# Optimization experiments

Measured on AMD Instinct MI355X. Metric: run time of the kernel, lower is better.

Reference implementation:

```python
import jax, jax.numpy as jnp
import numpy as np

VOCAB, EMBED, HIDDEN, NCLS, PAD = 50257, 512, 1024, 4, 0

def setup_inputs() -> dict:
    key = jax.random.key(0)
    k1, k2, k3, k4, k5, k6 = jax.random.split(key, 6)
    emb = jax.random.uniform(k1, (VOCAB, EMBED), jnp.float32, -0.1, 0.1)
    emb = emb.at[PAD].set(0.0)
    W = jax.random.normal(k2, (HIDDEN, EMBED), jnp.float32) * (2.0 / (EMBED + HIDDEN)) ** 0.5
    b_w = jnp.zeros((HIDDEN,), jnp.float32)
    U = jax.random.normal(k3, (HIDDEN, HIDDEN), jnp.float32) * (1.0 / HIDDEN) ** 0.5
    V = jax.random.normal(k4, (NCLS, HIDDEN), jnp.float32) * (2.0 / (HIDDEN + NCLS)) ** 0.5
    b_v = jnp.zeros((NCLS,), jnp.float32)
    x = jax.random.randint(k5, (64, 512), 0, VOCAB, jnp.int32)
    return {"x": x, "emb": emb, "W": W, "b_w": b_w, "U": U, "V": V, "b_v": b_v}

def reference(x, emb, W, b_w, U, V, b_v):
    # x: [B, S] int tokens. Dropouts are identity (eval mode).
    embedded = emb[x]                      # [B, S, E]
    # Precompute Wx for all timesteps in one GEMM: [B, S, H]
    wx = jnp.einsum('bse,he->bsh', embedded, W) + b_w
    B = x.shape[0]
    h0 = jnp.zeros((B, W.shape[0]), embedded.dtype)

    def step(h, wx_t):
        h = jnp.tanh(wx_t + h @ U.T)       # [B, H]
        return h, None

    h_final, _ = jax.lax.scan(step, h0, jnp.swapaxes(wx, 0, 1))  # scan over S
    return h_final @ V.T + b_v             # [B, NCLS]
```

## Files before the change

kernel.cpp:

```cpp
#include <hip/hip_runtime.h>
#include <stdint.h>

#define B 64
#define S 512
#define E 512
#define H 1024
#define NCLS 4

typedef __attribute__((ext_vector_type(8))) short short8;
typedef __attribute__((ext_vector_type(4))) float f32x4;

__device__ __forceinline__ unsigned short f32_to_bf16(float f) {
    unsigned int x = __float_as_uint(f);
    unsigned int r = (x + 0x7fffu + ((x >> 16) & 1u)) >> 16;
    return (unsigned short)r;
}
__device__ __forceinline__ float bf16_to_f32(unsigned short u) {
    return __uint_as_float(((unsigned int)u) << 16);
}

__device__ __forceinline__ void store_sc4u(unsigned int* p, unsigned int v) {
    asm volatile("global_store_dword %0, %1, off sc0 sc1"
                 :: "v"(p), "v"(v) : "memory");
}

#define K1_LDA 40

__global__ __launch_bounds__(256) void k_wx_gemm(
    const int* __restrict__ x, const float* __restrict__ emb,
    const float* __restrict__ W, const float* __restrict__ bw,
    unsigned short* __restrict__ wx)
{
    __shared__ unsigned short Asub[128 * K1_LDA];
    __shared__ unsigned short Bsub[128 * K1_LDA];

    const int t  = threadIdx.x;
    const int mt = blockIdx.x;
    const int nt = blockIdx.y;
    const int i0 = mt * 128;
    const int j0 = nt * 128;

    const int r  = t >> 1;
    const int kh = (t & 1) * 16;
    const int tok = x[i0 + r];
    const float* arow = emb + (size_t)tok * E;
    const float* brow = W + (size_t)(j0 + r) * E;

    const int lane = t & 63;
    const int w    = t >> 6;
    const int wm   = (w >> 1) * 64;
    const int wn   = (w & 1) * 64;
    const int fr   = lane & 15;
    const int kg   = lane >> 4;

    f32x4 acc[4][4] = {};

    for (int kt = 0; kt < E; kt += 32) {
        __syncthreads();
        {
            union { unsigned short us[8]; uint4 v; } p;
            const float* srcA = arow + kt + kh;
            #pragma unroll
            for (int i = 0; i < 8; ++i) p.us[i] = f32_to_bf16(srcA[i]);
            *(uint4*)&Asub[r * K1_LDA + kh] = p.v;
            #pragma unroll
            for (int i = 0; i < 8; ++i) p.us[i] = f32_to_bf16(srcA[8 + i]);
            *(uint4*)&Asub[r * K1_LDA + kh + 8] = p.v;
            const float* srcB = brow + kt + kh;
            #pragma unroll
            for (int i = 0; i < 8; ++i) p.us[i] = f32_to_bf16(srcB[i]);
            *(uint4*)&Bsub[r * K1_LDA + kh] = p.v;
            #pragma unroll
            for (int i = 0; i < 8; ++i) p.us[i] = f32_to_bf16(srcB[8 + i]);
            *(uint4*)&Bsub[r * K1_LDA + kh + 8] = p.v;
        }
        __syncthreads();

        short8 a[4], b[4];
        #pragma unroll
        for (int mi = 0; mi < 4; ++mi)
            a[mi] = *(const short8*)&Asub[(wm + mi * 16 + fr) * K1_LDA + kg * 8];
        #pragma unroll
        for (int ni = 0; ni < 4; ++ni)
            b[ni] = *(const short8*)&Bsub[(wn + ni * 16 + fr) * K1_LDA + kg * 8];
        #pragma unroll
        for (int mi = 0; mi < 4; ++mi)
            #pragma unroll
            for (int ni = 0; ni < 4; ++ni)
                acc[mi][ni] = __builtin_amdgcn_mfma_f32_16x16x32_bf16(
                                  a[mi], b[ni], acc[mi][ni], 0, 0, 0);
    }

    float bwv[4];
    #pragma unroll
    for (int ni = 0; ni < 4; ++ni) bwv[ni] = bw[j0 + wn + ni * 16 + fr];
    #pragma unroll
    for (int mi = 0; mi < 4; ++mi) {
        #pragma unroll
        for (int ni = 0; ni < 4; ++ni) {
            const int gn = j0 + wn + ni * 16 + fr;
            #pragma unroll
            for (int rr = 0; rr < 4; ++rr) {
                const int gm = i0 + wm + mi * 16 + kg * 4 + rr;
                const int bb = gm >> 9;
                const int ss = gm & 511;
                wx[(size_t)(ss * B + bb) * H + gn] =
                    f32_to_bf16(acc[mi][ni][rr] + bwv[ni]);
            }
        }
    }
}

__global__ __launch_bounds__(256) void k_rnn(
    const unsigned short* __restrict__ wx, const float* __restrict__ U,
    const float* __restrict__ Vw, const float* __restrict__ bv,
    unsigned int* __restrict__ hbuf, unsigned int* __restrict__ flags,
    float* __restrict__ out)
{
    __shared__ __align__(16) unsigned short Uhi[32 * 1024];
    __shared__ __align__(16) unsigned int Hh32[8 * 512];
    __shared__ __align__(16) unsigned int Hl32[8 * 512];
    __shared__ __align__(16) float redC[1024];

    const int t   = threadIdx.x;
    const int g   = blockIdx.x & 7;
    const int m   = blockIdx.x >> 3;
    const int j0  = m * 32;
    const int bg0 = g * 8;

    for (int rr = 0; rr < 32; ++rr) {
        f32x4 v = *(const f32x4*)(U + (size_t)(j0 + rr) * H + t * 4);
        uint2 hwd;
        hwd.x = f32_to_bf16(v[0]) | ((unsigned)f32_to_bf16(v[1]) << 16);
        hwd.y = f32_to_bf16(v[2]) | ((unsigned)f32_to_bf16(v[3]) << 16);
        const int byteoff = (rr * 2048 + t * 8) ^ ((rr & 7) << 4);
        *(uint2*)((char*)Uhi + byteoff) = hwd;
    }

    const int lane  = t & 63;
    const int w     = t >> 6;
    const int fr    = lane & 15;
    const int kg    = lane >> 4;
    const int kbase = w * 256;
    const int abrow = fr & 7;
    const int ob    = t >> 5;
    const int oj    = t & 31;

    unsigned int* fl = flags + g * 32;

    float wxv = bf16_to_f32(wx[(size_t)(bg0 + ob) * H + j0 + oj]);

    __syncthreads();

    for (int ts = 0; ts < S; ++ts) {
        const unsigned int* hr = hbuf + (ts & 1) * (B * H);
        unsigned int*       hw = hbuf + ((ts + 1) & 1) * (B * H);

        {
            const unsigned int* fp = fl + w * 8 + (lane & 7);
            unsigned int fv;
            do {
                fv = __hip_atomic_load(fp, __ATOMIC_RELAXED,
                                       __HIP_MEMORY_SCOPE_AGENT);
            } while (!__all((int)(fv >= (unsigned)ts)));
        }

        float wx_next = 0.f;
        if (ts + 1 < S)
            wx_next = bf16_to_f32(wx[(size_t)((ts + 1) * B + bg0 + ob) * H + j0 + oj]);

        {
            const unsigned long long* hb64 = (const unsigned long long*)hr;
            unsigned long long vv[16];
            #pragma unroll
            for (int i = 0; i < 16; ++i) {
                const int li = lane + 64 * i;
                const int b = li >> 7, col = li & 127;
                vv[i] = __hip_atomic_load(
                    hb64 + (size_t)(bg0 + b) * 512 + w * 128 + col,
                    __ATOMIC_RELAXED, __HIP_MEMORY_SCOPE_AGENT);
            }
            #pragma unroll
            for (int i = 0; i < 16; ++i) {
                const int li = lane + 64 * i;
                const int b = li >> 7;
                const int k2 = w * 128 + (li & 127);
                const unsigned int v0 = (unsigned int)vv[i];
                const unsigned int v1 = (unsigned int)(vv[i] >> 32);
                const int idx = (b * 512 + k2) ^ (b << 2);
                Hh32[idx] = (v0 >> 16) | (v1 & 0xffff0000u);
                Hl32[idx] = (v0 & 0xffffu) | (v1 << 16);
            }
        }

        f32x4 acc0 = {}, acc1 = {};
        #pragma unroll
        for (int kk = 0; kk < 8; ++kk) {
            const int k  = kbase + kk * 32 + kg * 8;
            const int ab = (abrow * 2048 + k * 2) ^ (abrow << 4);
            const short8 ahi = *(const short8*)((const char*)Hh32 + ab);
            const short8 alo = *(const short8*)((const char*)Hl32 + ab);
            const int b0 = (fr * 2048 + k * 2) ^ ((fr & 7) << 4);
            const int b1 = ((16 + fr) * 2048 + k * 2) ^ ((fr & 7) << 4);
            const short8 bh0 = *(const short8*)((const char*)Uhi + b0);
            const short8 bh1 = *(const short8*)((const char*)Uhi + b1);
            acc0 = __builtin_amdgcn_mfma_f32_16x16x32_bf16(ahi, bh0, acc0, 0, 0, 0);
            acc0 = __builtin_amdgcn_mfma_f32_16x16x32_bf16(alo, bh0, acc0, 0, 0, 0);
            acc1 = __builtin_amdgcn_mfma_f32_16x16x32_bf16(ahi, bh1, acc1, 0, 0, 0);
            acc1 = __builtin_amdgcn_mfma_f32_16x16x32_bf16(alo, bh1, acc1, 0, 0, 0);
        }

        if (kg < 2) {
            #pragma unroll
            for (int rr = 0; rr < 4; ++rr) {
                const int mb = kg * 4 + rr;
                redC[w * 256 + mb * 32 + fr]      = acc0[rr];
                redC[w * 256 + mb * 32 + 16 + fr] = acc1[rr];
            }
        }
        __syncthreads();

        float sum = redC[      ob * 32 + oj] + redC[256 + ob * 32 + oj]
                  + redC[512 + ob * 32 + oj] + redC[768 + ob * 32 + oj];

        float p = wxv + sum;
        p = fminf(fmaxf(p, -15.f), 15.f);
        const float e  = __expf(2.0f * p);
        const float hv = 1.0f - 2.0f / (e + 1.0f);

        const unsigned short hib = f32_to_bf16(hv);
        const unsigned short lob = f32_to_bf16(hv - bf16_to_f32(hib));
        store_sc4u(hw + (size_t)(bg0 + ob) * H + j0 + oj,
                   ((unsigned int)hib << 16) | lob);
        asm volatile("s_waitcnt vmcnt(0)" ::: "memory");
        __syncthreads();
        if (t == 0)
            __hip_atomic_store(&fl[m], (unsigned)(ts + 1), __ATOMIC_RELAXED,
                               __HIP_MEMORY_SCOPE_AGENT);
        wxv = wx_next;
    }

    if (m == 0) {
        if (t < 32)
            while (__hip_atomic_load(&fl[t], __ATOMIC_RELAXED,
                                     __HIP_MEMORY_SCOPE_AGENT) < (unsigned)S) {}
        __syncthreads();
        const unsigned int* hf = hbuf;
        const int o = t & 31, part = t >> 5;
        const int pb = o >> 2, c = o & 3;
        const unsigned long long* hrow =
            (const unsigned long long*)(hf + (size_t)(bg0 + pb) * H) + part * 64;
        const float* vrow = Vw + (size_t)c * H + part * 128;
        float partial = 0.f;
        for (int q = 0; q < 64; ++q) {
            unsigned long long vvq = __hip_atomic_load(hrow + q, __ATOMIC_RELAXED,
                                                       __HIP_MEMORY_SCOPE_AGENT);
            const unsigned int v0 = (unsigned int)vvq;
            const unsigned int v1 = (unsigned int)(vvq >> 32);
            const float h0 = bf16_to_f32((unsigned short)(v0 >> 16))
                           + bf16_to_f32((unsigned short)(v0 & 0xffffu));
            const float h1 = bf16_to_f32((unsigned short)(v1 >> 16))
                           + bf16_to_f32((unsigned short)(v1 & 0xffffu));
            partial += h0 * vrow[2 * q] + h1 * vrow[2 * q + 1];
        }
        __syncthreads();
        redC[part * 32 + o] = partial;
        __syncthreads();
        if (t < 32) {
            float sv = 0.f;
            #pragma unroll
            for (int pq = 0; pq < 8; ++pq) sv += redC[pq * 32 + t];
            out[(bg0 + (t >> 2)) * NCLS + (t & 3)] = sv + bv[t & 3];
        }
    }
}

extern "C" void kernel_launch(void* const* d_in, const int* in_sizes, int n_in,
                              void* d_out, int out_size, void* d_ws, size_t ws_size,
                              hipStream_t stream)
{
    const int*   x   = (const int*)d_in[0];
    const float* emb = (const float*)d_in[1];
    const float* W   = (const float*)d_in[2];
    const float* bw  = (const float*)d_in[3];
    const float* U   = (const float*)d_in[4];
    const float* V   = (const float*)d_in[5];
    const float* bv  = (const float*)d_in[6];
    float* out = (float*)d_out;

    unsigned short* wx = (unsigned short*)d_ws;
    const size_t WX_BYTES = (size_t)S * B * H * sizeof(unsigned short);
    unsigned int* hbuf = (unsigned int*)((char*)d_ws + WX_BYTES);
    const size_t HB_BYTES = (size_t)2 * B * H * sizeof(unsigned int);
    unsigned int* flags = (unsigned int*)((char*)d_ws + WX_BYTES + HB_BYTES);

    hipMemsetAsync((char*)d_ws + WX_BYTES, 0, HB_BYTES + 2048, stream);

    hipLaunchKernelGGL(k_wx_gemm, dim3(256, 8), dim3(256), 0, stream,
                       x, emb, W, bw, wx);
    hipLaunchKernelGGL(k_rnn, dim3(256), dim3(256), 0, stream,
                       wx, U, V, bv, hbuf, flags, out);
}
```

Baseline: 1.592 ms.

## Load hidden state directly into MFMA registers, skipping the LDS staging

Each step now reads the previous hidden state from global memory with 128-bit coherent loads straight into each lane's MFMA A-operand layout. The hi/lo bf16 halves are split in registers instead of being written to and read back from the Hh32/Hl32 shared buffers. The wx prefetch is moved ahead of the flag spin-wait so it overlaps the wait. A dummy LDS pad array is added, apparently to limit occupancy or block placement. The trade-off is that lanes with fr>=8 sit idle during the loads, and their A rows stay uninitialised.

Result: slower. 1.759 ms (+10.5%).

```diff
diff --git a/kernel.cpp b/kernel.cpp
--- a/kernel.cpp
+++ b/kernel.cpp
@@ -23,6 +23,10 @@
     asm volatile("global_store_dword %0, %1, off sc0 sc1"
                  :: "v"(p), "v"(v) : "memory");
 }
+
+#define LD128(dst, base, off) \
+    asm volatile("global_load_dwordx4 %0, %1, off offset:" #off " sc0 sc1" \
+                 : "=&v"(dst) : "v"(base) : "memory")
 
 #define K1_LDA 40
 
@@ -118,15 +122,16 @@
     float* __restrict__ out)
 {
     __shared__ __align__(16) unsigned short Uhi[32 * 1024];
-    __shared__ __align__(16) unsigned int Hh32[8 * 512];
-    __shared__ __align__(16) unsigned int Hl32[8 * 512];
     __shared__ __align__(16) float redC[1024];
+    __shared__ __align__(16) unsigned int pad_lds[8192];
 
     const int t   = threadIdx.x;
     const int g   = blockIdx.x & 7;
     const int m   = blockIdx.x >> 3;
     const int j0  = m * 32;
     const int bg0 = g * 8;
+
+    ((volatile unsigned int*)pad_lds)[t] = (unsigned int)t;
 
     for (int rr = 0; rr < 32; ++rr) {
         f32x4 v = *(const f32x4*)(U + (size_t)(j0 + rr) * H + t * 4);
@@ -156,6 +161,10 @@
         const unsigned int* hr = hbuf + (ts & 1) * (B * H);
         unsigned int*       hw = hbuf + ((ts + 1) & 1) * (B * H);
 
+        float wx_next = 0.f;
+        if (ts + 1 < S)
+            wx_next = bf16_to_f32(wx[(size_t)((ts + 1) * B + bg0 + ob) * H + j0 + oj]);
+
         {
             const unsigned int* fp = fl + w * 8 + (lane & 7);
             unsigned int fv;
@@ -165,49 +174,45 @@
             } while (!__all((int)(fv >= (unsigned)ts)));
         }
 
-        float wx_next = 0.f;
-        if (ts + 1 < S)
-            wx_next = bf16_to_f32(wx[(size_t)((ts + 1) * B + bg0 + ob) * H + j0 + oj]);
-
+        uint4 hv[16];
         {
-            const unsigned long long* hb64 = (const unsigned long long*)hr;
-            unsigned long long vv[16];
-            #pragma unroll
-            for (int i = 0; i < 16; ++i) {
-                const int li = lane + 64 * i;
-                const int b = li >> 7, col = li & 127;
-                vv[i] = __hip_atomic_load(
-                    hb64 + (size_t)(bg0 + b) * 512 + w * 128 + col,
-                    __ATOMIC_RELAXED, __HIP_MEMORY_SCOPE_AGENT);
+            const unsigned int* hb =
+                hr + (size_t)(bg0 + abrow) * H + kbase + kg * 8;
+            if (fr < 8) {
+                LD128(hv[ 0], hb,   0); LD128(hv[ 1], hb,  16);
+                LD128(hv[ 2], hb, 128); LD128(hv[ 3], hb, 144);
+                LD128(hv[ 4], hb, 256); LD128(hv[ 5], hb, 272);
+                LD128(hv[ 6], hb, 384); LD128(hv[ 7], hb, 400);
+                LD128(hv[ 8], hb, 512); LD128(hv[ 9], hb, 528);
+                LD128(hv[10], hb, 640); LD128(hv[11], hb, 656);
+                LD128(hv[12], hb, 768); LD128(hv[13], hb, 784);
+                LD128(hv[14], hb, 896); LD128(hv[15], hb, 912);
             }
-            #pragma unroll
-            for (int i = 0; i < 16; ++i) {
-                const int li = lane + 64 * i;
-                const int b = li >> 7;
-                const int k2 = w * 128 + (li & 127);
-                const unsigned int v0 = (unsigned int)vv[i];
-                const unsigned int v1 = (unsigned int)(vv[i] >> 32);
-                const int idx = (b * 512 + k2) ^ (b << 2);
-                Hh32[idx] = (v0 >> 16) | (v1 & 0xffff0000u);
-                Hl32[idx] = (v0 & 0xffffu) | (v1 << 16);
+            asm volatile("s_waitcnt vmcnt(0)" ::: "memory");
+            __builtin_amdgcn_sched_barrier(0);
+        }
+
+        f32x4 acc0 = {}, acc1 = {};
+        #pragma unroll
+        for (int kk = 0; kk < 8; ++kk) {
+            const uint4 pa = hv[2 * kk], pb = hv[2 * kk + 1];
+            const unsigned int wj[8] = {pa.x, pa.y, pa.z, pa.w,
+                                        pb.x, pb.y, pb.z, pb.w};
+            union { unsigned int u[4]; short8 s; } Ahi, Alo;
+            #pragma unroll
+            for (int i = 0; i < 4; ++i) {
+                Ahi.u[i] = (wj[2*i+1] & 0xffff0000u) | (wj[2*i] >> 16);
+                Alo.u[i] = (wj[2*i+1] << 16) | (wj[2*i] & 0xffffu);
             }
-        }
-
-        f32x4 acc0 = {}, acc1 = {};
-        #pragma unroll
-        for (int kk = 0; kk < 8; ++kk) {
             const int k  = kbase + kk * 32 + kg * 8;
-            const int ab = (abrow * 2048 + k * 2) ^ (abrow << 4);
-            const short8 ahi = *(const short8*)((const char*)Hh32 + ab);
-            const short8 alo = *(const short8*)((const char*)Hl32 + ab);
             const int b0 = (fr * 2048 + k * 2) ^ ((fr & 7) << 4);
             const int b1 = ((16 + fr) * 2048 + k * 2) ^ ((fr & 7) << 4);
             const short8 bh0 = *(const short8*)((const char*)Uhi + b0);
             const short8 bh1 = *(const short8*)((const char*)Uhi + b1);
-            acc0 = __builtin_amdgcn_mfma_f32_16x16x32_bf16(ahi, bh0, acc0, 0, 0, 0);
-            acc0 = __builtin_amdgcn_mfma_f32_16x16x32_bf16(alo, bh0, acc0, 0, 0, 0);
-            acc1 = __builtin_amdgcn_mfma_f32_16x16x32_bf16(ahi, bh1, acc1, 0, 0, 0);
-            acc1 = __builtin_amdgcn_mfma_f32_16x16x32_bf16(alo, bh1, acc1, 0, 0, 0);
+            acc0 = __builtin_amdgcn_mfma_f32_16x16x32_bf16(Ahi.s, bh0, acc0, 0, 0, 0);
+            acc0 = __builtin_amdgcn_mfma_f32_16x16x32_bf16(Alo.s, bh0, acc0, 0, 0, 0);
+            acc1 = __builtin_amdgcn_mfma_f32_16x16x32_bf16(Ahi.s, bh1, acc1, 0, 0, 0);
+            acc1 = __builtin_amdgcn_mfma_f32_16x16x32_bf16(Alo.s, bh1, acc1, 0, 0, 0);
         }
 
         if (kg < 2) {
@@ -226,10 +231,10 @@
         float p = wxv + sum;
         p = fminf(fmaxf(p, -15.f), 15.f);
         const float e  = __expf(2.0f * p);
-        const float hv = 1.0f - 2.0f / (e + 1.0f);
-
-        const unsigned short hib = f32_to_bf16(hv);
-        const unsigned short lob = f32_to_bf16(hv - bf16_to_f32(hib));
+        const float hv2 = 1.0f - 2.0f / (e + 1.0f);
+
+        const unsigned short hib = f32_to_bf16(hv2);
+        const unsigned short lob = f32_to_bf16(hv2 - bf16_to_f32(hib));
         store_sc4u(hw + (size_t)(bg0 + ob) * H + j0 + oj,
                    ((unsigned int)hib << 16) | lob);
         asm volatile("s_waitcnt vmcnt(0)" ::: "memory");
```
